# Kernel tuning notes

Measured on AMD Instinct MI355X. Metric: run time of the kernel, lower is better.

The kernel has to match this reference:

```python
import jax, jax.numpy as jnp
import numpy as np

BS, DIM, HID, T = 4096, 64, 256, 101
GAMMA = 0.1
EPS = 1e-12  # pinverse guard for the 1x1 matrix G G^T


def setup_inputs() -> dict:
    key = jax.random.key(0)
    k0, k1, k2, k3 = jax.random.split(key, 4)
    return {
        "y0": jax.random.normal(k0, (BS, DIM), dtype=jnp.float32),
        "t": jnp.linspace(0.0, 1.0, T).astype(jnp.float32),
        "W1": jax.random.normal(k1, (DIM, HID), dtype=jnp.float32) * 0.05,
        "b1": jnp.zeros((HID,), dtype=jnp.float32),
        "W2": jax.random.normal(k2, (HID, DIM), dtype=jnp.float32) * 0.05,
        "b2": jnp.zeros((DIM,), dtype=jnp.float32),
        "wg": jax.random.normal(k3, (DIM,), dtype=jnp.float32) * 0.1,
        "bg": jnp.zeros((), dtype=jnp.float32),
    }


def reference(y0, t, W1, b1, W2, b2, wg, bg):
    # f_model: 2-layer tanh MLP (ignores t, as is common for autonomous dynamics)
    def f_model(ti, u):
        return jnp.tanh(u @ W1 + b1) @ W2 + b2  # (bs, dim)

    # g_fn: scalar constraint per sample
    def g_single(ui):
        return jnp.tanh(ui @ wg + bg)  # scalar

    def dynamic(ti, u):
        f_u = f_model(ti, u)                              # (bs, dim)
        g_u = jax.vmap(g_single)(u)                       # (bs,)
        # Torch detaches u before autograd Jacobian (create_graph keeps param path)
        G = jax.vmap(jax.grad(g_single))(jax.lax.stop_gradient(u))  # (bs, dim) == G_u row
        # F_u = G^T (G G^T)^+ ; G G^T is 1x1 -> scalar pinverse
        s = jnp.sum(G * G, axis=-1)                       # (bs,)
        pinv = jnp.where(jnp.abs(s) > EPS, 1.0 / s, 0.0)  # (bs,)
        stable = GAMMA * (g_u * pinv)[:, None] * G        # (bs, dim)
        return f_u - stable

    dt = t[1] - t[0]  # Euler solver uses constant dt

    def step(y, ti):
        y_new = y + dynamic(ti, y) * dt
        return y_new, y_new

    _, ys = jax.lax.scan(step, y0, t[:-1])
    return jnp.concatenate([y0[None], ys], axis=0)  # (T, bs, dim)
```

## Files before the change

kernel.cpp:

```cpp
#include <hip/hip_runtime.h>


#define GAMMA 0.1f
#define EPSG  1e-12f

typedef __attribute__((ext_vector_type(8))) short bf16x8;
typedef __attribute__((ext_vector_type(4))) float f32x4;

__device__ __forceinline__ float ftanh(float x) {
    float e = __expf(2.0f * x);
    return 1.0f - 2.0f * __builtin_amdgcn_rcpf(e + 1.0f);
}

__device__ __forceinline__ unsigned int f2bf(float f) {
    unsigned int u = __float_as_uint(f);
    return (u + 0x7fffu + ((u >> 16) & 1u)) >> 16;
}

#define BARRIER_LGKM() asm volatile("s_waitcnt lgkmcnt(0)\ns_barrier" ::: "memory")

__global__ __launch_bounds__(512, 1) void snde_kernel(
    const float* __restrict__ y0, const float* __restrict__ t,
    const float* __restrict__ W1, const float* __restrict__ b1,
    const float* __restrict__ W2, const float* __restrict__ b2,
    const float* __restrict__ wg, const float* __restrict__ bgp,
    float* __restrict__ out)
{
    __shared__ unsigned short uAs[16 * 64];
    __shared__ unsigned short hAs[16 * 256];
    __shared__ float          fpart[8][16][68];

    const int tid = threadIdx.x;
    const int w   = tid >> 6;
    const int l   = tid & 63;
    const int l15 = l & 15;
    const int lg  = l >> 4;
    const int s0g = blockIdx.x * 16;

    bf16x8 B1[2][2];
    #pragma unroll
    for (int nt = 0; nt < 2; ++nt) {
        const int n = w * 32 + nt * 16 + l15;
        #pragma unroll
        for (int kt = 0; kt < 2; ++kt) {
            bf16x8 v;
            #pragma unroll
            for (int j = 0; j < 8; ++j) {
                const int k = kt * 32 + lg * 8 + j;
                v[j] = (short)f2bf(W1[k * 256 + n]);
            }
            B1[nt][kt] = v;
        }
    }
    bf16x8 B2[4];
    #pragma unroll
    for (int nt = 0; nt < 4; ++nt) {
        const int n = nt * 16 + l15;
        bf16x8 v;
        #pragma unroll
        for (int j = 0; j < 8; ++j) {
            const int k = w * 32 + lg * 8 + j;
            v[j] = (short)f2bf(W2[k * 64 + n]);
        }
        B2[nt] = v;
    }

    float b1v[2];
    #pragma unroll
    for (int nt = 0; nt < 2; ++nt) b1v[nt] = b1[w * 32 + nt * 16 + l15];

    const int sU = tid >> 5;
    const int dd = (tid & 31) * 2;
    const float2 wg2  = *(const float2*)(&wg[dd]);
    const float2 b2v2 = *(const float2*)(&b2[dd]);
    float wsum = wg2.x * wg2.x + wg2.y * wg2.y;
    #pragma unroll
    for (int m = 1; m < 32; m <<= 1) wsum += __shfl_xor(wsum, m, 64);
    const float bg  = bgp[0];
    const float dtv = t[1] - t[0];

    float2 uv;
    {
        uv = *(const float2*)(&y0[(size_t)(s0g + sU) * 64 + dd]);
        unsigned int p0 = f2bf(uv.x) | (f2bf(uv.y) << 16);
        unsigned int off = (((unsigned)(sU * 128 + dd * 2)) ^ ((unsigned)(sU & 7) << 4)) >> 2;
        ((unsigned int*)uAs)[off] = p0;
        *(float2*)(&out[(size_t)(s0g + sU) * 64 + dd]) = uv;
    }
    __syncthreads();

    for (int step = 0; step < 100; ++step) {
        float coef;
        {
            float zp = uv.x * wg2.x + uv.y * wg2.y;
            #pragma unroll
            for (int m = 1; m < 32; m <<= 1) zp += __shfl_xor(zp, m, 64);
            const float th = ftanh(zp + bg);
            const float q  = 1.0f - th * th;
            const float sg = q * q * wsum;
            const float pinv = (fabsf(sg) > EPSG) ? __builtin_amdgcn_rcpf(sg) : 0.0f;
            coef = GAMMA * th * pinv * q;
        }

        bf16x8 A1[2];
        #pragma unroll
        for (int kt = 0; kt < 2; ++kt) {
            unsigned int boff = ((unsigned)(l15 * 128 + (kt * 32 + lg * 8) * 2))
                              ^ ((unsigned)(l15 & 7) << 4);
            A1[kt] = *(const bf16x8*)((const char*)uAs + boff);
        }
        f32x4 acc1[2];
        #pragma unroll
        for (int nt = 0; nt < 2; ++nt) {
            acc1[nt][0] = b1v[nt]; acc1[nt][1] = b1v[nt];
            acc1[nt][2] = b1v[nt]; acc1[nt][3] = b1v[nt];
        }
        #pragma unroll
        for (int nt = 0; nt < 2; ++nt)
            #pragma unroll
            for (int kt = 0; kt < 2; ++kt)
                acc1[nt] = __builtin_amdgcn_mfma_f32_16x16x32_bf16(A1[kt], B1[nt][kt], acc1[nt], 0, 0, 0);

        #pragma unroll
        for (int nt = 0; nt < 2; ++nt) {
            const int n = w * 32 + nt * 16 + l15;
            #pragma unroll
            for (int i = 0; i < 4; ++i) {
                const int m = lg * 4 + i;
                const float th = ftanh(acc1[nt][i]);
                unsigned int boff = ((unsigned)(m * 512 + n * 2)) ^ ((unsigned)(m & 7) << 4);
                *(unsigned short*)((char*)hAs + boff) = (unsigned short)f2bf(th);
            }
        }

        bf16x8 A2;
        {
            unsigned int boff = ((unsigned)(l15 * 512 + (w * 32 + lg * 8) * 2))
                              ^ ((unsigned)(l15 & 7) << 4);
            A2 = *(const bf16x8*)((const char*)hAs + boff);
        }
        f32x4 acc2[4];
        #pragma unroll
        for (int nt = 0; nt < 4; ++nt) {
            acc2[nt][0] = 0.f; acc2[nt][1] = 0.f; acc2[nt][2] = 0.f; acc2[nt][3] = 0.f;
        }
        #pragma unroll
        for (int nt = 0; nt < 4; ++nt)
            acc2[nt] = __builtin_amdgcn_mfma_f32_16x16x32_bf16(A2, B2[nt], acc2[nt], 0, 0, 0);

        #pragma unroll
        for (int nt = 0; nt < 4; ++nt) {
            const int n = nt * 16 + l15;
            #pragma unroll
            for (int i = 0; i < 4; ++i)
                fpart[w][lg * 4 + i][n] = acc2[nt][i];
        }
        BARRIER_LGKM();

        {
            float2 fs = {0.f, 0.f};
            #pragma unroll
            for (int p = 0; p < 8; ++p) {
                const float2 fp = *(const float2*)(&fpart[p][sU][dd]);
                fs.x += fp.x; fs.y += fp.y;
            }
            float2 un;
            un.x = uv.x + (fs.x + b2v2.x - coef * wg2.x) * dtv;
            un.y = uv.y + (fs.y + b2v2.y - coef * wg2.y) * dtv;
            uv = un;
            unsigned int p0 = f2bf(un.x) | (f2bf(un.y) << 16);
            unsigned int off = (((unsigned)(sU * 128 + dd * 2)) ^ ((unsigned)(sU & 7) << 4)) >> 2;
            ((unsigned int*)uAs)[off] = p0;
            *(float2*)(&out[(size_t)(step + 1) * (4096 * 64) + (size_t)(s0g + sU) * 64 + dd]) = un;
        }
        BARRIER_LGKM();
    }
}

extern "C" void kernel_launch(void* const* d_in, const int* in_sizes, int n_in,
                              void* d_out, int out_size, void* d_ws, size_t ws_size,
                              hipStream_t stream) {
    const float* y0 = (const float*)d_in[0];
    const float* t  = (const float*)d_in[1];
    const float* W1 = (const float*)d_in[2];
    const float* b1 = (const float*)d_in[3];
    const float* W2 = (const float*)d_in[4];
    const float* b2 = (const float*)d_in[5];
    const float* wg = (const float*)d_in[6];
    const float* bg = (const float*)d_in[7];
    float* out = (float*)d_out;

    snde_kernel<<<dim3(256), dim3(512), 0, stream>>>(y0, t, W1, b1, W2, b2, wg, bg, out);
}
```

Baseline: 107.5 us.

## Split work into 8-sample blocks of 4 waves to double grid size

Each block now handles 8 samples with 256 threads instead of 16 samples with 512, and the launch grid doubles to 512 blocks. Each wave therefore covers a wider slice of the hidden dimension: more MFMAs per wave, and fewer partial sums in shared memory for the cross-wave reduction. The 16-row MFMA tiles are only half filled, since the upper rows are zero-padded and their writes are masked. The aim is to spread work across more CUs on mi355x (256 CUs) and cut barrier and reduction cost. In exchange, half of the MFMA throughput goes to padding.

```diff
diff --git a/kernel.cpp b/kernel.cpp
--- a/kernel.cpp
+++ b/kernel.cpp
@@ -19,7 +19,7 @@
 
 #define BARRIER_LGKM() asm volatile("s_waitcnt lgkmcnt(0)\ns_barrier" ::: "memory")
 
-__global__ __launch_bounds__(512, 1) void snde_kernel(
+__global__ __launch_bounds__(256, 2) void snde_kernel(
     const float* __restrict__ y0, const float* __restrict__ t,
     const float* __restrict__ W1, const float* __restrict__ b1,
     const float* __restrict__ W2, const float* __restrict__ b2,
@@ -28,19 +28,19 @@
 {
     __shared__ unsigned short uAs[16 * 64];
     __shared__ unsigned short hAs[16 * 256];
-    __shared__ float          fpart[8][16][68];
+    __shared__ float          fpart[4][8][68];
 
     const int tid = threadIdx.x;
     const int w   = tid >> 6;
     const int l   = tid & 63;
     const int l15 = l & 15;
     const int lg  = l >> 4;
-    const int s0g = blockIdx.x * 16;
-
-    bf16x8 B1[2][2];
-    #pragma unroll
-    for (int nt = 0; nt < 2; ++nt) {
-        const int n = w * 32 + nt * 16 + l15;
+    const int s0g = blockIdx.x * 8;
+
+    bf16x8 B1[4][2];
+    #pragma unroll
+    for (int nt = 0; nt < 4; ++nt) {
+        const int n = w * 64 + nt * 16 + l15;
         #pragma unroll
         for (int kt = 0; kt < 2; ++kt) {
             bf16x8 v;
@@ -52,22 +52,25 @@
             B1[nt][kt] = v;
         }
     }
-    bf16x8 B2[4];
-    #pragma unroll
-    for (int nt = 0; nt < 4; ++nt) {
-        const int n = nt * 16 + l15;
-        bf16x8 v;
-        #pragma unroll
-        for (int j = 0; j < 8; ++j) {
-            const int k = w * 32 + lg * 8 + j;
-            v[j] = (short)f2bf(W2[k * 64 + n]);
-        }
-        B2[nt] = v;
-    }
-
-    float b1v[2];
-    #pragma unroll
-    for (int nt = 0; nt < 2; ++nt) b1v[nt] = b1[w * 32 + nt * 16 + l15];
+    bf16x8 B2[2][4];
+    #pragma unroll
+    for (int kt = 0; kt < 2; ++kt) {
+        #pragma unroll
+        for (int nt = 0; nt < 4; ++nt) {
+            const int n = nt * 16 + l15;
+            bf16x8 v;
+            #pragma unroll
+            for (int j = 0; j < 8; ++j) {
+                const int k = w * 64 + kt * 32 + lg * 8 + j;
+                v[j] = (short)f2bf(W2[k * 64 + n]);
+            }
+            B2[kt][nt] = v;
+        }
+    }
+
+    float b1v[4];
+    #pragma unroll
+    for (int nt = 0; nt < 4; ++nt) b1v[nt] = b1[w * 64 + nt * 16 + l15];
 
     const int sU = tid >> 5;
     const int dd = (tid & 31) * 2;
@@ -79,11 +82,17 @@
     const float bg  = bgp[0];
     const float dtv = t[1] - t[0];
 
+    ((unsigned int*)uAs)[tid]       = 0u;
+    ((unsigned int*)uAs)[tid + 256] = 0u;
+    #pragma unroll
+    for (int j = 0; j < 8; ++j) ((unsigned int*)hAs)[tid + 256 * j] = 0u;
+    __syncthreads();
+
     float2 uv;
     {
         uv = *(const float2*)(&y0[(size_t)(s0g + sU) * 64 + dd]);
         unsigned int p0 = f2bf(uv.x) | (f2bf(uv.y) << 16);
-        unsigned int off = (((unsigned)(sU * 128 + dd * 2)) ^ ((unsigned)(sU & 7) << 4)) >> 2;
+        unsigned int off = (((unsigned)(sU * 128 + dd * 2)) ^ ((unsigned)sU << 4)) >> 2;
         ((unsigned int*)uAs)[off] = p0;
         *(float2*)(&out[(size_t)(s0g + sU) * 64 + dd]) = uv;
     }
@@ -109,35 +118,38 @@
                               ^ ((unsigned)(l15 & 7) << 4);
             A1[kt] = *(const bf16x8*)((const char*)uAs + boff);
         }
-        f32x4 acc1[2];
-        #pragma unroll
-        for (int nt = 0; nt < 2; ++nt) {
+        f32x4 acc1[4];
+        #pragma unroll
+        for (int nt = 0; nt < 4; ++nt) {
             acc1[nt][0] = b1v[nt]; acc1[nt][1] = b1v[nt];
             acc1[nt][2] = b1v[nt]; acc1[nt][3] = b1v[nt];
         }
         #pragma unroll
-        for (int nt = 0; nt < 2; ++nt)
+        for (int nt = 0; nt < 4; ++nt)
             #pragma unroll
             for (int kt = 0; kt < 2; ++kt)
                 acc1[nt] = __builtin_amdgcn_mfma_f32_16x16x32_bf16(A1[kt], B1[nt][kt], acc1[nt], 0, 0, 0);
 
-        #pragma unroll
-        for (int nt = 0; nt < 2; ++nt) {
-            const int n = w * 32 + nt * 16 + l15;
-            #pragma unroll
-            for (int i = 0; i < 4; ++i) {
-                const int m = lg * 4 + i;
-                const float th = ftanh(acc1[nt][i]);
-                unsigned int boff = ((unsigned)(m * 512 + n * 2)) ^ ((unsigned)(m & 7) << 4);
-                *(unsigned short*)((char*)hAs + boff) = (unsigned short)f2bf(th);
-            }
-        }
-
-        bf16x8 A2;
-        {
-            unsigned int boff = ((unsigned)(l15 * 512 + (w * 32 + lg * 8) * 2))
-                              ^ ((unsigned)(l15 & 7) << 4);
-            A2 = *(const bf16x8*)((const char*)hAs + boff);
+        if (lg < 2) {
+            #pragma unroll
+            for (int nt = 0; nt < 4; ++nt) {
+                const int n = w * 64 + nt * 16 + l15;
+                #pragma unroll
+                for (int i = 0; i < 4; ++i) {
+                    const int m = lg * 4 + i;
+                    const float th = ftanh(acc1[nt][i]);
+                    unsigned int boff = ((unsigned)(m * 512 + n * 2)) ^ ((unsigned)(m & 7) << 4);
+                    *(unsigned short*)((char*)hAs + boff) = (unsigned short)f2bf(th);
+                }
+            }
+        }
+
+        bf16x8 A2[2];
+        #pragma unroll
+        for (int kt = 0; kt < 2; ++kt) {
+            const int kb = w * 64 + kt * 32 + lg * 8;
+            unsigned int boff = ((unsigned)(l15 * 512 + kb * 2)) ^ ((unsigned)(l15 & 7) << 4);
+            A2[kt] = *(const bf16x8*)((const char*)hAs + boff);
         }
         f32x4 acc2[4];
         #pragma unroll
@@ -146,21 +158,25 @@
         }
         #pragma unroll
         for (int nt = 0; nt < 4; ++nt)
-            acc2[nt] = __builtin_amdgcn_mfma_f32_16x16x32_bf16(A2, B2[nt], acc2[nt], 0, 0, 0);
-
-        #pragma unroll
-        for (int nt = 0; nt < 4; ++nt) {
-            const int n = nt * 16 + l15;
-            #pragma unroll
-            for (int i = 0; i < 4; ++i)
-                fpart[w][lg * 4 + i][n] = acc2[nt][i];
+            #pragma unroll
+            for (int kt = 0; kt < 2; ++kt)
+                acc2[nt] = __builtin_amdgcn_mfma_f32_16x16x32_bf16(A2[kt], B2[kt][nt], acc2[nt], 0, 0, 0);
+
+        if (lg < 2) {
+            #pragma unroll
+            for (int nt = 0; nt < 4; ++nt) {
+                const int n = nt * 16 + l15;
+                #pragma unroll
+                for (int i = 0; i < 4; ++i)
+                    fpart[w][lg * 4 + i][n] = acc2[nt][i];
+            }
         }
         BARRIER_LGKM();
 
         {
             float2 fs = {0.f, 0.f};
             #pragma unroll
-            for (int p = 0; p < 8; ++p) {
+            for (int p = 0; p < 4; ++p) {
                 const float2 fp = *(const float2*)(&fpart[p][sU][dd]);
                 fs.x += fp.x; fs.y += fp.y;
             }
@@ -169,7 +185,7 @@
             un.y = uv.y + (fs.y + b2v2.y - coef * wg2.y) * dtv;
             uv = un;
             unsigned int p0 = f2bf(un.x) | (f2bf(un.y) << 16);
-            unsigned int off = (((unsigned)(sU * 128 + dd * 2)) ^ ((unsigned)(sU & 7) << 4)) >> 2;
+            unsigned int off = (((unsigned)(sU * 128 + dd * 2)) ^ ((unsigned)sU << 4)) >> 2;
             ((unsigned int*)uAs)[off] = p0;
             *(float2*)(&out[(size_t)(step + 1) * (4096 * 64) + (size_t)(s0g + sU) * 64 + dd]) = un;
         }
@@ -190,5 +206,5 @@
     const float* bg = (const float*)d_in[7];
     float* out = (float*)d_out;
 
-    snde_kernel<<<dim3(256), dim3(512), 0, stream>>>(y0, t, W1, b1, W2, b2, wg, bg, out);
-}
+    snde_kernel<<<dim3(512), dim3(256), 0, stream>>>(y0, t, W1, b1, W2, b2, wg, bg, out);
+}
```

Result: slower. 136.6 us (+27.1%).

## Fold constraint dot product into MFMA and pack partial sums as bf16 pairs

Applied to the files above, without the earlier changes.

The per-sample u·wg reduction, previously done with a five-level cross-lane shuffle, is now computed by an extra MFMA on wave 0 against a wg column and passed through shared memory. The eight per-wave partial outputs of the second layer are stored as packed bf16 pairs in a swizzled buffer instead of fp32, halving LDS write and read traffic. Each thread now owns two strided dims instead of an adjacent pair, so global stores become scalar and strided. This lowers reduction precision to bf16 for the partial sums and for the constraint dot product, and adds a serial dependency on wave 0.

```diff
diff --git a/kernel.cpp b/kernel.cpp
--- a/kernel.cpp
+++ b/kernel.cpp
@@ -15,6 +15,13 @@
 __device__ __forceinline__ unsigned int f2bf(float f) {
     unsigned int u = __float_as_uint(f);
     return (u + 0x7fffu + ((u >> 16) & 1u)) >> 16;
+}
+
+__device__ __forceinline__ float bflo(unsigned int p) {
+    return __uint_as_float(p << 16);
+}
+__device__ __forceinline__ float bfhi(unsigned int p) {
+    return __uint_as_float(p & 0xffff0000u);
 }
 
 #define BARRIER_LGKM() asm volatile("s_waitcnt lgkmcnt(0)\ns_barrier" ::: "memory")
@@ -28,7 +35,8 @@
 {
     __shared__ unsigned short uAs[16 * 64];
     __shared__ unsigned short hAs[16 * 256];
-    __shared__ float          fpart[8][16][68];
+    __shared__ unsigned int   fpp[8 * 16 * 32];
+    __shared__ float          zs[16];
 
     const int tid = threadIdx.x;
     const int w   = tid >> 6;
@@ -64,44 +72,49 @@
         }
         B2[nt] = v;
     }
+    bf16x8 Bz[2];
+    #pragma unroll
+    for (int kt = 0; kt < 2; ++kt) {
+        bf16x8 v;
+        #pragma unroll
+        for (int j = 0; j < 8; ++j) {
+            const int k = kt * 32 + lg * 8 + j;
+            v[j] = (l15 == 0) ? (short)f2bf(wg[k]) : (short)0;
+        }
+        Bz[kt] = v;
+    }
 
     float b1v[2];
     #pragma unroll
     for (int nt = 0; nt < 2; ++nt) b1v[nt] = b1[w * 32 + nt * 16 + l15];
 
     const int sU = tid >> 5;
-    const int dd = (tid & 31) * 2;
-    const float2 wg2  = *(const float2*)(&wg[dd]);
-    const float2 b2v2 = *(const float2*)(&b2[dd]);
-    float wsum = wg2.x * wg2.x + wg2.y * wg2.y;
+    const int q  = tid & 31;
+    const int hi = q >> 4;
+    const int e  = q & 15;
+    const int d0 = 32 * hi + e;
+    const int d1 = d0 + 16;
+    const float wg_0 = wg[d0], wg_1 = wg[d1];
+    const float b2_0 = b2[d0], b2_1 = b2[d1];
+    float wsum = wg_0 * wg_0 + wg_1 * wg_1;
     #pragma unroll
     for (int m = 1; m < 32; m <<= 1) wsum += __shfl_xor(wsum, m, 64);
     const float bg  = bgp[0];
     const float dtv = t[1] - t[0];
 
-    float2 uv;
+    float uv0 = y0[(size_t)(s0g + sU) * 64 + d0];
+    float uv1 = y0[(size_t)(s0g + sU) * 64 + d1];
     {
-        uv = *(const float2*)(&y0[(size_t)(s0g + sU) * 64 + dd]);
-        unsigned int p0 = f2bf(uv.x) | (f2bf(uv.y) << 16);
-        unsigned int off = (((unsigned)(sU * 128 + dd * 2)) ^ ((unsigned)(sU & 7) << 4)) >> 2;
-        ((unsigned int*)uAs)[off] = p0;
-        *(float2*)(&out[(size_t)(s0g + sU) * 64 + dd]) = uv;
+        unsigned int b0 = ((unsigned)(sU * 128 + d0 * 2)) ^ ((unsigned)(sU & 7) << 4);
+        unsigned int b1o = ((unsigned)(sU * 128 + d1 * 2)) ^ ((unsigned)(sU & 7) << 4);
+        *(unsigned short*)((char*)uAs + b0)  = (unsigned short)f2bf(uv0);
+        *(unsigned short*)((char*)uAs + b1o) = (unsigned short)f2bf(uv1);
+        out[(size_t)(s0g + sU) * 64 + d0] = uv0;
+        out[(size_t)(s0g + sU) * 64 + d1] = uv1;
     }
     __syncthreads();
 
     for (int step = 0; step < 100; ++step) {
-        float coef;
-        {
-            float zp = uv.x * wg2.x + uv.y * wg2.y;
-            #pragma unroll
-            for (int m = 1; m < 32; m <<= 1) zp += __shfl_xor(zp, m, 64);
-            const float th = ftanh(zp + bg);
-            const float q  = 1.0f - th * th;
-            const float sg = q * q * wsum;
-            const float pinv = (fabsf(sg) > EPSG) ? __builtin_amdgcn_rcpf(sg) : 0.0f;
-            coef = GAMMA * th * pinv * q;
-        }
-
         bf16x8 A1[2];
         #pragma unroll
         for (int kt = 0; kt < 2; ++kt) {
@@ -120,6 +133,14 @@
             #pragma unroll
             for (int kt = 0; kt < 2; ++kt)
                 acc1[nt] = __builtin_amdgcn_mfma_f32_16x16x32_bf16(A1[kt], B1[nt][kt], acc1[nt], 0, 0, 0);
+
+        if (w == 0) {
+            f32x4 accz = {0.f, 0.f, 0.f, 0.f};
+            #pragma unroll
+            for (int kt = 0; kt < 2; ++kt)
+                accz = __builtin_amdgcn_mfma_f32_16x16x32_bf16(A1[kt], Bz[kt], accz, 0, 0, 0);
+            if (l15 == 0) *(f32x4*)(&zs[lg * 4]) = accz;
+        }
 
         #pragma unroll
         for (int nt = 0; nt < 2; ++nt) {
@@ -149,29 +170,41 @@
             acc2[nt] = __builtin_amdgcn_mfma_f32_16x16x32_bf16(A2, B2[nt], acc2[nt], 0, 0, 0);
 
         #pragma unroll
-        for (int nt = 0; nt < 4; ++nt) {
-            const int n = nt * 16 + l15;
-            #pragma unroll
-            for (int i = 0; i < 4; ++i)
-                fpart[w][lg * 4 + i][n] = acc2[nt][i];
+        for (int i = 0; i < 4; ++i) {
+            const int s = lg * 4 + i;
+            const unsigned sw = ((unsigned)(s & 7)) << 2;
+            fpp[w * 512 + s * 32 + (((unsigned)l15) ^ sw)] =
+                f2bf(acc2[0][i]) | (f2bf(acc2[1][i]) << 16);
+            fpp[w * 512 + s * 32 + (((unsigned)(16 + l15)) ^ sw)] =
+                f2bf(acc2[2][i]) | (f2bf(acc2[3][i]) << 16);
         }
         BARRIER_LGKM();
 
         {
-            float2 fs = {0.f, 0.f};
+            const unsigned idxr = ((unsigned)(hi * 16 + e)) ^ (((unsigned)(sU & 7)) << 2);
+            float fs0 = 0.f, fs1 = 0.f;
             #pragma unroll
             for (int p = 0; p < 8; ++p) {
-                const float2 fp = *(const float2*)(&fpart[p][sU][dd]);
-                fs.x += fp.x; fs.y += fp.y;
+                const unsigned int pk = fpp[p * 512 + sU * 32 + idxr];
+                fs0 += bflo(pk);
+                fs1 += bfhi(pk);
             }
-            float2 un;
-            un.x = uv.x + (fs.x + b2v2.x - coef * wg2.x) * dtv;
-            un.y = uv.y + (fs.y + b2v2.y - coef * wg2.y) * dtv;
-            uv = un;
-            unsigned int p0 = f2bf(un.x) | (f2bf(un.y) << 16);
-            unsigned int off = (((unsigned)(sU * 128 + dd * 2)) ^ ((unsigned)(sU & 7) << 4)) >> 2;
-            ((unsigned int*)uAs)[off] = p0;
-            *(float2*)(&out[(size_t)(step + 1) * (4096 * 64) + (size_t)(s0g + sU) * 64 + dd]) = un;
+            const float zp = zs[sU];
+            const float th = ftanh(zp + bg);
+            const float qq = 1.0f - th * th;
+            const float sg = qq * qq * wsum;
+            const float pinv = (fabsf(sg) > EPSG) ? __builtin_amdgcn_rcpf(sg) : 0.0f;
+            const float coef = GAMMA * th * pinv * qq;
+            const float un0 = uv0 + (fs0 + b2_0 - coef * wg_0) * dtv;
+            const float un1 = uv1 + (fs1 + b2_1 - coef * wg_1) * dtv;
+            uv0 = un0; uv1 = un1;
+            unsigned int b0 = ((unsigned)(sU * 128 + d0 * 2)) ^ ((unsigned)(sU & 7) << 4);
+            unsigned int b1o = ((unsigned)(sU * 128 + d1 * 2)) ^ ((unsigned)(sU & 7) << 4);
+            *(unsigned short*)((char*)uAs + b0)  = (unsigned short)f2bf(un0);
+            *(unsigned short*)((char*)uAs + b1o) = (unsigned short)f2bf(un1);
+            float* orow = &out[(size_t)(step + 1) * (4096 * 64) + (size_t)(s0g + sU) * 64];
+            orow[d0] = un0;
+            orow[d1] = un1;
         }
         BARRIER_LGKM();
     }
```

New measurement: 110.4 us. 2.7% more time.
